# Performance work log

Measured on AMD Instinct MI355X. Metric: run time of the kernel, lower is better.

Reference implementation:

```python
import jax, jax.numpy as jnp
import numpy as np

H, C, OC, WIN = 12, 768, 768, 4
HD = C // H  # 64
B, T = 4, 1024


def setup_inputs() -> dict:
    key = jax.random.key(0)
    ks = jax.random.split(key, 8)
    s = C ** -0.5  # xavier-ish scale for 1x1 convs
    rel_s = HD ** -0.5
    return {
        "x": jax.random.normal(ks[0], (B, C, T), jnp.float32),
        "c": jax.random.normal(ks[1], (B, C, T), jnp.float32),
        "mask": jnp.ones((B, 1, T, T), jnp.float32),
        "wq": jax.random.normal(ks[2], (C, C), jnp.float32) * s,
        "bq": jnp.zeros((C,), jnp.float32),
        "wk": jax.random.normal(ks[3], (C, C), jnp.float32) * s,
        "bk": jnp.zeros((C,), jnp.float32),
        "wv": jax.random.normal(ks[4], (C, C), jnp.float32) * s,
        "bv": jnp.zeros((C,), jnp.float32),
        "wo": jax.random.normal(ks[5], (OC, C), jnp.float32) * s,
        "bo": jnp.zeros((OC,), jnp.float32),
        "emb_rel_k": jax.random.normal(ks[6], (H, 2 * WIN + 1, HD), jnp.float32) * rel_s,
        "emb_rel_v": jax.random.normal(ks[7], (H, 2 * WIN + 1, HD), jnp.float32) * rel_s,
    }


def _conv1x1(x, w, b):
    # Conv1d(kernel_size=1): pointwise linear over channels. x:(b,c,t) w:(o,c)
    return jnp.einsum('oc,bct->bot', w, x) + b[None, :, None]


def _get_rel_emb(emb, t):
    pad = max(t - WIN, 0)
    start = max(WIN + 1 - t, 0)
    emb = jnp.pad(emb, ((0, 0), (pad, pad), (0, 0)))
    return emb[:, start:start + 2 * t - 1, :]


def _rel_to_abs(x):
    # (b,h,t,2t-1) -> (b,h,t,t) via the pad/reshape skew trick
    b, h, t, _ = x.shape
    x = jnp.pad(x, ((0, 0), (0, 0), (0, 0), (0, 1))).reshape(b, h, 2 * t * t)
    x = jnp.pad(x, ((0, 0), (0, 0), (0, t - 1))).reshape(b, h, t + 1, 2 * t - 1)
    return x[:, :, :t, t - 1:]


def _abs_to_rel(x):
    # (b,h,t,t) -> (b,h,t,2t-1) via inverse skew trick
    b, h, t, _ = x.shape
    x = jnp.pad(x, ((0, 0), (0, 0), (0, 0), (0, t - 1))).reshape(b, h, t * (2 * t - 1))
    x = jnp.pad(x, ((0, 0), (0, 0), (t, 0))).reshape(b, h, t, 2 * t)
    return x[:, :, :, 1:]


def reference(x, c, mask, wq, bq, wk, bk, wv, bv, wo, bo, emb_rel_k, emb_rel_v):
    b, _, t = x.shape
    scale = HD ** -0.5
    # (b,c,t) -> (b,h,t,hd)
    q = _conv1x1(x, wq, bq).reshape(b, H, HD, t).transpose(0, 1, 3, 2)
    k = _conv1x1(c, wk, bk).reshape(b, H, HD, t).transpose(0, 1, 3, 2)
    v = _conv1x1(c, wv, bv).reshape(b, H, HD, t).transpose(0, 1, 3, 2)
    scores = jnp.einsum('bhqd,bhkd->bhqk', q, k) * scale  # (b,h,t,t)
    rel_k = _get_rel_emb(emb_rel_k, t)                    # (h,2t-1,d)
    rel_logits = jnp.einsum('bhtd,hmd->bhtm', q, rel_k)   # (b,h,t,2t-1)
    scores = scores + _rel_to_abs(rel_logits) * scale
    scores = jnp.where(mask == 0, jnp.float32(-1e4), scores)
    attn = jax.nn.softmax(scores, axis=-1)
    out = jnp.einsum('bhqk,bhkd->bhqd', attn, v)
    rel_v = _get_rel_emb(emb_rel_v, t)
    out = out + jnp.einsum('bhtm,hmd->bhtd', _abs_to_rel(attn), rel_v)
    out = out.transpose(0, 1, 3, 2).reshape(b, C, t)      # (b,c,t)
    return _conv1x1(out, wo, bo)
```

## Files before the change

kernel.cpp:

```cpp
#include <hip/hip_runtime.h>
#include <stdint.h>
#include <stddef.h>

#define B_ 4
#define T_ 1024
#define C_ 768
#define H_ 12
#define QSCALE 0.18033688011112042f
#define MASKPEN -14427.0f

typedef __attribute__((ext_vector_type(4))) float f32x4;
typedef __attribute__((ext_vector_type(8))) short s16x8;
typedef __attribute__((ext_vector_type(4))) float float4v;

typedef const __attribute__((address_space(1))) uint32_t ga_u32;
typedef __attribute__((address_space(3))) uint32_t lds_u32;

__device__ __forceinline__ float bf2f(uint16_t u) {
    union { uint32_t u; float f; } cv; cv.u = ((uint32_t)u) << 16; return cv.f;
}
__device__ __forceinline__ uint16_t f2bf(float f) {
    union { float f; uint32_t u; } cv; cv.f = f;
    uint32_t u = cv.u;
    return (uint16_t)((u + 0x7FFFu + ((u >> 16) & 1u)) >> 16);
}
__device__ __forceinline__ uint16_t f2bf_trunc(float f) {
    union { float f; uint32_t u; } cv; cv.f = f;
    return (uint16_t)(cv.u >> 16);
}
__device__ __forceinline__ void gload16(const uint16_t* g, uint16_t* l) {
    __builtin_amdgcn_global_load_lds((ga_u32*)g, (lds_u32*)l, 16, 0, 0);
}

__global__ void transpose_bf16_kernel(const float* __restrict__ x,
                                      const float* __restrict__ c,
                                      uint16_t* __restrict__ xT,
                                      uint16_t* __restrict__ cT) {
    __shared__ float tile[32][33];
    const int which = blockIdx.z;
    const int b = blockIdx.y;
    const int t0 = (blockIdx.x % (T_ / 32)) * 32;
    const int c0 = (blockIdx.x / (T_ / 32)) * 32;
    const float* src = (which ? c : x) + (size_t)b * C_ * T_;
    uint16_t* dst = (which ? cT : xT) + (size_t)b * T_ * C_;
    const int lj = threadIdx.x & 31, li = threadIdx.x >> 5;
    #pragma unroll
    for (int i = li; i < 32; i += 8)
        tile[i][lj] = src[(size_t)(c0 + i) * T_ + t0 + lj];
    __syncthreads();
    #pragma unroll
    for (int i = li; i < 32; i += 8)
        dst[(size_t)(t0 + i) * C_ + c0 + lj] = f2bf(tile[lj][i]);
}

__global__ void convert_weights_kernel(const float* __restrict__ wq,
                                       const float* __restrict__ wk,
                                       const float* __restrict__ wv,
                                       const float* __restrict__ wo,
                                       uint16_t* __restrict__ out) {
    const int which = blockIdx.y;
    const float* w = (which == 0) ? wq : (which == 1) ? wk : (which == 2) ? wv : wo;
    const float sc = (which == 0) ? QSCALE : 1.0f;
    uint16_t* dst = out + (size_t)which * C_ * C_;
    const int i = (blockIdx.x * 256 + threadIdx.x) * 4;
    float4v v = *(const float4v*)(w + i);
    uint32_t lo = (uint32_t)f2bf(v[0] * sc) | ((uint32_t)f2bf(v[1] * sc) << 16);
    uint32_t hi = (uint32_t)f2bf(v[2] * sc) | ((uint32_t)f2bf(v[3] * sc) << 16);
    uint32_t* d32 = (uint32_t*)(dst + i);
    d32[0] = lo; d32[1] = hi;
}

__global__ void convert_ek_kernel(const float* __restrict__ ek,
                                  uint16_t* __restrict__ ekb) {
    const int i = blockIdx.x * 256 + threadIdx.x;
    ekb[i] = f2bf(ek[i]);
}

__global__ void mask_bits_kernel(const float* __restrict__ mask,
                                 uint32_t* __restrict__ bits) {
    const size_t i = (size_t)blockIdx.x * 256 + threadIdx.x;
    const float m = mask[i];
    unsigned long long bal = __ballot(m != 0.0f);
    const int lane = threadIdx.x & 63;
    if (lane == 0)       bits[i >> 5] = (uint32_t)bal;
    else if (lane == 32) bits[i >> 5] = (uint32_t)(bal >> 32);
}

__global__ void mask_flags_kernel(const uint32_t* __restrict__ bits,
                                  uint32_t* __restrict__ flags) {
    const int b = blockIdx.y, i0 = blockIdx.x * 64;
    const uint32_t* p = bits + ((size_t)b * T_ + i0) * 32;
    bool ok = true;
    #pragma unroll
    for (int it = 0; it < 8; ++it) ok &= (p[it * 256 + threadIdx.x] == 0xFFFFFFFFu);
    __shared__ int s_ok[4];
    const bool wall = __all(ok);
    if ((threadIdx.x & 63) == 0) s_ok[threadIdx.x >> 6] = wall ? 1 : 0;
    __syncthreads();
    if (threadIdx.x == 0)
        flags[b * 16 + blockIdx.x] = (uint32_t)(s_ok[0] & s_ok[1] & s_ok[2] & s_ok[3]);
}

template <bool OPROJ>
__global__ __launch_bounds__(256, 2)
void gemm_kernel(const uint16_t* __restrict__ xT, const uint16_t* __restrict__ cT,
                 const uint16_t* __restrict__ wb,
                 const float* __restrict__ bq, const float* __restrict__ bk,
                 const float* __restrict__ bv, const float* __restrict__ bo,
                 const uint16_t* __restrict__ attT,
                 uint16_t* __restrict__ Qb, uint16_t* __restrict__ Kb,
                 uint16_t* __restrict__ Vb, float* __restrict__ outp) {
    const int tid = threadIdx.x;
    const int z = blockIdx.z;

    const uint16_t* A; const uint16_t* Bm; const float* bias;
    uint16_t* Cb = nullptr; float* Cf = nullptr;
    int N, ldc; bool bias_col; float bscale = 1.0f;
    if (!OPROJ) {
        const int bat = z & 3, which = z >> 2;
        if (which == 0) {
            A = xT + (size_t)bat * T_ * C_; Bm = wb;                bias = bq;
            Cb = Qb + (size_t)bat * T_ * C_; N = C_; ldc = C_; bias_col = true;
            bscale = QSCALE;
        } else if (which == 1) {
            A = cT + (size_t)bat * T_ * C_; Bm = wb + 1 * C_ * C_;  bias = bk;
            Cb = Kb + (size_t)bat * T_ * C_; N = C_; ldc = C_; bias_col = true;
        } else {
            A = wb + 2 * (size_t)C_ * C_;   Bm = cT + (size_t)(z & 3) * T_ * C_; bias = bv;
            Cb = Vb + (size_t)bat * C_ * T_; N = T_; ldc = T_; bias_col = false;
        }
    } else {
        A = wb + 3 * (size_t)C_ * C_; Bm = attT + (size_t)z * T_ * C_; bias = bo;
        Cf = outp + (size_t)z * C_ * T_; N = T_; ldc = T_; bias_col = false;
    }
    const int tn_cnt = N / 128;
    const int tm = blockIdx.x / tn_cnt, tn = blockIdx.x % tn_cnt;
    const int row0 = tm * 128, col0 = tn * 128;

    __shared__ uint16_t As[128 * 64];
    __shared__ uint16_t Bs[128 * 64];

    const int w = tid >> 6, l = tid & 63;
    const int wr = w & 1, wc = w >> 1;

    const f32x4 zz = {0.f, 0.f, 0.f, 0.f};
    f32x4 acc[4][4];
    #pragma unroll
    for (int i = 0; i < 4; ++i)
        #pragma unroll
        for (int j = 0; j < 4; ++j) acc[i][j] = zz;

    const int sr = tid >> 3, sp = tid & 7;

    for (int kt = 0; kt < 12; ++kt) {
        const int k0 = kt * 64;
        #pragma unroll
        for (int it = 0; it < 4; ++it) {
            const int row = it * 32 + sr;
            const int cch = sp ^ (row & 7);
            gload16(A + (size_t)(row0 + row) * 768 + k0 + cch * 8, &As[row * 64 + sp * 8]);
        }
        #pragma unroll
        for (int it = 0; it < 4; ++it) {
            const int row = it * 32 + sr;
            const int cch = sp ^ (row & 7);
            gload16(Bm + (size_t)(col0 + row) * 768 + k0 + cch * 8, &Bs[row * 64 + sp * 8]);
        }
        __syncthreads();

        #pragma unroll
        for (int kk = 0; kk < 2; ++kk) {
            s16x8 af[4], bf[4];
            #pragma unroll
            for (int i = 0; i < 4; ++i) {
                const int arow = wr * 64 + i * 16 + (l & 15);
                const int ach = (kk * 4 + (l >> 4)) ^ (arow & 7);
                af[i] = *(const s16x8*)(&As[arow * 64 + ach * 8]);
                const int brow = wc * 64 + i * 16 + (l & 15);
                const int bch = (kk * 4 + (l >> 4)) ^ (brow & 7);
                bf[i] = *(const s16x8*)(&Bs[brow * 64 + bch * 8]);
            }
            #pragma unroll
            for (int i = 0; i < 4; ++i)
                #pragma unroll
                for (int j = 0; j < 4; ++j)
                    acc[i][j] = __builtin_amdgcn_mfma_f32_16x16x32_bf16(af[i], bf[j], acc[i][j], 0, 0, 0);
        }
        __syncthreads();
    }

    #pragma unroll
    for (int i = 0; i < 4; ++i) {
        const int rowb = row0 + wr * 64 + i * 16 + ((l >> 4) * 4);
        #pragma unroll
        for (int j = 0; j < 4; ++j) {
            const int col = col0 + wc * 64 + j * 16 + (l & 15);
            const float bc = bias_col ? bias[col] * bscale : 0.f;
            #pragma unroll
            for (int r = 0; r < 4; ++r) {
                const int row = rowb + r;
                const float v = acc[i][j][r] + (bias_col ? bc : bias[row]);
                if (!OPROJ) Cb[(size_t)row * ldc + col] = f2bf(v);
                else        Cf[(size_t)row * ldc + col] = v;
            }
        }
    }
}

__global__ __launch_bounds__(256, 2)
void attn_kernel(const uint16_t* __restrict__ Qb, const uint16_t* __restrict__ Kb,
                 const uint16_t* __restrict__ Vb, const uint32_t* __restrict__ mbits,
                 const uint32_t* __restrict__ flags,
                 const uint16_t* __restrict__ ekb, const float* __restrict__ emb_v,
                 uint16_t* __restrict__ attT) {
    const int i0 = blockIdx.x * 64;
    const int h = blockIdx.y, b = blockIdx.z;
    const int tid = threadIdx.x, w = tid >> 6, l = tid & 63;

    __shared__ uint16_t Ks[2][64 * 64];
    __shared__ uint16_t Vs[2][64 * 64];
    __shared__ uint16_t Ps[64 * 72];
    __shared__ uint16_t Es[16 * 72];
    __shared__ float rk[64 * 9];
    __shared__ float sband[64 * 9];

    const uint16_t* Kbase = Kb + (size_t)b * T_ * C_ + h * 64;
    const uint16_t* Vbase = Vb + (size_t)b * C_ * T_ + (size_t)(h * 64) * T_;
    const int sr = tid >> 3, sp = tid & 7;

    auto stage = [&](int jt, int buf) {
        const int j0s = jt * 64;
        #pragma unroll
        for (int it = 0; it < 2; ++it) {
            const int row = it * 32 + sr;
            const int cch = sp ^ (row & 7);
            gload16(Kbase + (size_t)(j0s + row) * C_ + cch * 8, &Ks[buf][row * 64 + sp * 8]);
        }
        #pragma unroll
        for (int it = 0; it < 2; ++it) {
            const int row = it * 32 + sr;
            const int cch = sp ^ (row & 7);
            gload16(Vbase + (size_t)row * T_ + j0s + cch * 8, &Vs[buf][row * 64 + sp * 8]);
        }
    };

    stage(0, 0);

    s16x8 qf[2];
    {
        const int row = i0 + w * 16 + (l & 15);
        const uint16_t* qp = Qb + ((size_t)(b * T_ + row)) * C_ + h * 64 + (l >> 4) * 8;
        qf[0] = *(const s16x8*)(qp);
        qf[1] = *(const s16x8*)(qp + 32);
    }

    {
        const int idx = tid * 4;
        const int row = idx >> 6, col = idx & 63;
        uint64_t val = 0;
        if (row < 9) val = *(const uint64_t*)(ekb + ((size_t)h * 9 + row) * 64 + col);
        *(uint64_t*)&Es[row * 72 + col] = val;
    }
    for (int t = tid; t < 64 * 9; t += 256) sband[t] = -1e30f;
    __syncthreads();

    {
        f32x4 racc = {0.f, 0.f, 0.f, 0.f};
        #pragma unroll
        for (int kk = 0; kk < 2; ++kk) {
            s16x8 ef = *(const s16x8*)(&Es[(l & 15) * 72 + (l >> 4) * 8 + kk * 32]);
            racc = __builtin_amdgcn_mfma_f32_16x16x32_bf16(qf[kk], ef, racc, 0, 0, 0);
        }
        if ((l & 15) < 9) {
            #pragma unroll
            for (int r = 0; r < 4; ++r)
                rk[(w * 16 + (l >> 4) * 4 + r) * 9 + (l & 15)] = racc[r];
        }
    }

    const bool maskones = (flags[b * 16 + blockIdx.x] != 0);
    const uint32_t* mrow = mbits + (size_t)b * T_ * 32;

    float m[4], lsum[4];
    const f32x4 zz = {0.f, 0.f, 0.f, 0.f};
    f32x4 oacc[4] = {zz, zz, zz, zz};
    #pragma unroll
    for (int r = 0; r < 4; ++r) { m[r] = -1e30f; lsum[r] = 0.f; }

    const int iMin = i0 + w * 16, iMax = iMin + 15;

    for (int jt = 0; jt < 16; ++jt) {
        const int cur = jt & 1;
        if (jt < 15) stage(jt + 1, cur ^ 1);
        const int j0 = jt * 64;

        float sv[4][4];
        #pragma unroll
        for (int tn = 0; tn < 4; ++tn) {
            f32x4 s = zz;
            #pragma unroll
            for (int kk = 0; kk < 2; ++kk) {
                const int krow = tn * 16 + (l & 15);
                const int kch = (kk * 4 + (l >> 4)) ^ (krow & 7);
                s16x8 kf = *(const s16x8*)(&Ks[cur][krow * 64 + kch * 8]);
                s = __builtin_amdgcn_mfma_f32_16x16x32_bf16(qf[kk], kf, s, 0, 0, 0);
            }
            #pragma unroll
            for (int r = 0; r < 4; ++r) sv[tn][r] = s[r];
        }

        const bool bandTile = (j0 <= iMax + 5) && (j0 + 63 >= iMin - 3);
        if (bandTile) {
            #pragma unroll
            for (int tn = 0; tn < 4; ++tn)
                #pragma unroll
                for (int r = 0; r < 4; ++r) {
                    const int iloc = w * 16 + (l >> 4) * 4 + r;
                    const int rr = (j0 + tn * 16 + (l & 15)) - (i0 + iloc) + 3;
                    if ((unsigned)rr < 9u) sv[tn][r] += rk[iloc * 9 + rr];
                }
        }
        if (!maskones) {
            #pragma unroll
            for (int r = 0; r < 4; ++r) {
                const int i = i0 + w * 16 + (l >> 4) * 4 + r;
                const uint32_t m0 = mrow[(size_t)i * 32 + (j0 >> 5)];
                const uint32_t m1 = mrow[(size_t)i * 32 + (j0 >> 5) + 1];
                #pragma unroll
                for (int tn = 0; tn < 4; ++tn) {
                    const uint32_t mw = (tn < 2) ? m0 : m1;
                    const int bit = (tn * 16 + (l & 15)) & 31;
                    if (!((mw >> bit) & 1u)) sv[tn][r] = MASKPEN;
                }
            }
        }
        if (bandTile) {
            #pragma unroll
            for (int tn = 0; tn < 4; ++tn)
                #pragma unroll
                for (int r = 0; r < 4; ++r) {
                    const int iloc = w * 16 + (l >> 4) * 4 + r;
                    const int rr = (j0 + tn * 16 + (l & 15)) - (i0 + iloc) + 3;
                    if ((unsigned)rr < 9u) sband[iloc * 9 + rr] = sv[tn][r];
                }
        }

        float mx[4];
        #pragma unroll
        for (int r = 0; r < 4; ++r)
            mx[r] = fmaxf(fmaxf(sv[0][r], sv[1][r]), fmaxf(sv[2][r], sv[3][r]));
        const bool need = (mx[0] > m[0]) | (mx[1] > m[1]) | (mx[2] > m[2]) | (mx[3] > m[3]);
        if (__any(need)) {
            #pragma unroll
            for (int r = 0; r < 4; ++r) {
                float v = mx[r];
                v = fmaxf(v, __shfl_xor(v, 1));
                v = fmaxf(v, __shfl_xor(v, 2));
                v = fmaxf(v, __shfl_xor(v, 4));
                v = fmaxf(v, __shfl_xor(v, 8));
                const float mn = fmaxf(m[r], v);
                const float alpha = exp2f(m[r] - mn);
                m[r] = mn;
                lsum[r] *= alpha;
                #pragma unroll
                for (int td = 0; td < 4; ++td) oacc[td][r] *= alpha;
            }
        }
        #pragma unroll
        for (int r = 0; r < 4; ++r) {
            #pragma unroll
            for (int tn = 0; tn < 4; ++tn) {
                const float p = exp2f(sv[tn][r] - m[r]);
                sv[tn][r] = p;
                lsum[r] += p;
            }
        }

        #pragma unroll
        for (int tn = 0; tn < 4; ++tn)
            #pragma unroll
            for (int r = 0; r < 4; ++r) {
                const int prow = w * 16 + (l >> 4) * 4 + r;
                Ps[prow * 72 + tn * 16 + (l & 15)] = f2bf_trunc(sv[tn][r]);
            }

        #pragma unroll
        for (int ks = 0; ks < 2; ++ks) {
            const int prow = w * 16 + (l & 15);
            s16x8 pf = *(const s16x8*)(&Ps[prow * 72 + ks * 32 + (l >> 4) * 8]);
            #pragma unroll
            for (int td = 0; td < 4; ++td) {
                const int vrow = td * 16 + (l & 15);
                const int vch = (ks * 4 + (l >> 4)) ^ (vrow & 7);
                s16x8 vf = *(const s16x8*)(&Vs[cur][vrow * 64 + vch * 8]);
                oacc[td] = __builtin_amdgcn_mfma_f32_16x16x32_bf16(pf, vf, oacc[td], 0, 0, 0);
            }
        }
        __syncthreads();
    }

    float invl[4];
    #pragma unroll
    for (int r = 0; r < 4; ++r) {
        float s = lsum[r];
        s += __shfl_xor(s, 1);
        s += __shfl_xor(s, 2);
        s += __shfl_xor(s, 4);
        s += __shfl_xor(s, 8);
        invl[r] = 1.f / s;
    }
    float ab[4][9];
    #pragma unroll
    for (int r = 0; r < 4; ++r) {
        const int iloc = w * 16 + (l >> 4) * 4 + r;
        #pragma unroll
        for (int rr = 0; rr < 9; ++rr)
            ab[r][rr] = exp2f(sband[iloc * 9 + rr] - m[r]) * invl[r];
    }
    #pragma unroll
    for (int td = 0; td < 4; ++td) {
        const int d = td * 16 + (l & 15);
        const float* ev = emb_v + (size_t)h * 9 * 64 + d;
        #pragma unroll
        for (int r = 0; r < 4; ++r) {
            float v = oacc[td][r] * invl[r];
            #pragma unroll
            for (int rr = 0; rr < 9; ++rr) v += ab[r][rr] * ev[rr * 64];
            const int i = i0 + w * 16 + (l >> 4) * 4 + r;
            attT[((size_t)(b * T_ + i)) * C_ + h * 64 + d] = f2bf(v);
        }
    }
}

extern "C" void kernel_launch(void* const* d_in, const int* in_sizes, int n_in,
                              void* d_out, int out_size, void* d_ws, size_t ws_size,
                              hipStream_t stream) {
    const float* x    = (const float*)d_in[0];
    const float* c    = (const float*)d_in[1];
    const float* mask = (const float*)d_in[2];
    const float* wq   = (const float*)d_in[3];
    const float* bq   = (const float*)d_in[4];
    const float* wk   = (const float*)d_in[5];
    const float* bk   = (const float*)d_in[6];
    const float* wv   = (const float*)d_in[7];
    const float* bv   = (const float*)d_in[8];
    const float* wo   = (const float*)d_in[9];
    const float* bo   = (const float*)d_in[10];
    const float* ek   = (const float*)d_in[11];
    const float* ev   = (const float*)d_in[12];
    float* out = (float*)d_out;

    uint8_t* ws = (uint8_t*)d_ws;
    size_t off = 0;
    auto alloc = [&](size_t bytes) {
        uint8_t* p = ws + off;
        off += (bytes + 255) & ~(size_t)255;
        return p;
    };
    uint16_t* xT   = (uint16_t*)alloc((size_t)B_ * T_ * C_ * 2);
    uint16_t* cT   = (uint16_t*)alloc((size_t)B_ * T_ * C_ * 2);
    uint16_t* wb   = (uint16_t*)alloc((size_t)4 * C_ * C_ * 2);
    uint16_t* Qb   = (uint16_t*)alloc((size_t)B_ * T_ * C_ * 2);
    uint16_t* Kb   = (uint16_t*)alloc((size_t)B_ * T_ * C_ * 2);
    uint16_t* Vb   = (uint16_t*)alloc((size_t)B_ * C_ * T_ * 2);
    uint16_t* attT = (uint16_t*)alloc((size_t)B_ * T_ * C_ * 2);
    uint32_t* mbits = (uint32_t*)alloc((size_t)B_ * T_ * 32 * 4);
    uint16_t* ekb  = (uint16_t*)alloc((size_t)H_ * 9 * 64 * 2);
    uint32_t* mflags = (uint32_t*)alloc((size_t)B_ * 16 * 4);

    transpose_bf16_kernel<<<dim3(768, B_, 2), 256, 0, stream>>>(x, c, xT, cT);
    convert_weights_kernel<<<dim3(576, 4), 256, 0, stream>>>(wq, wk, wv, wo, wb);
    convert_ek_kernel<<<dim3(27), 256, 0, stream>>>(ek, ekb);
    mask_bits_kernel<<<dim3((B_ * T_ * T_) / 256), 256, 0, stream>>>(mask, mbits);
    mask_flags_kernel<<<dim3(16, B_), 256, 0, stream>>>(mbits, mflags);
    gemm_kernel<false><<<dim3(48, 1, 12), 256, 0, stream>>>(xT, cT, wb, bq, bk, bv, bo,
                                                            attT, Qb, Kb, Vb, out);
    attn_kernel<<<dim3(T_ / 64, H_, B_), 256, 0, stream>>>(Qb, Kb, Vb, mbits, mflags,
                                                           ekb, ev, attT);
    gemm_kernel<true><<<dim3(48, 1, 4), 256, 0, stream>>>(xT, cT, wb, bq, bk, bv, bo,
                                                          attT, Qb, Kb, Vb, out);
}
```

Measured before the change: 220.9 us.

## Use 128-row query tiles with 512-thread attention blocks and remapped grid

The attention kernel now handles 128 query rows per block with 8 waves sharing each staged K/V tile, which halves the K/V global traffic per query. The grid is flattened to 384 blocks with a remapping that groups batch-head pairs, which may improve L2 locality. The mask-flag granularity is widened to 128 rows to match, and the input transpose kernel is vectorised to float4 loads and 64-bit packed stores. The larger blocks use more LDS and registers per block, so fewer blocks may be resident per CU, and only 384 blocks are launched.

```diff
diff --git a/kernel.cpp b/kernel.cpp
--- a/kernel.cpp
+++ b/kernel.cpp
@@ -39,18 +39,20 @@
     __shared__ float tile[32][33];
     const int which = blockIdx.z;
     const int b = blockIdx.y;
-    const int t0 = (blockIdx.x % (T_ / 32)) * 32;
-    const int c0 = (blockIdx.x / (T_ / 32)) * 32;
+    const int t0 = (blockIdx.x & 31) * 32;
+    const int c0 = (blockIdx.x >> 5) * 32;
     const float* src = (which ? c : x) + (size_t)b * C_ * T_;
     uint16_t* dst = (which ? cT : xT) + (size_t)b * T_ * C_;
-    const int lj = threadIdx.x & 31, li = threadIdx.x >> 5;
-    #pragma unroll
-    for (int i = li; i < 32; i += 8)
-        tile[i][lj] = src[(size_t)(c0 + i) * T_ + t0 + lj];
+    const int li = threadIdx.x >> 3, lj4 = (threadIdx.x & 7) * 4;
+    float4v v = *(const float4v*)(src + (size_t)(c0 + li) * T_ + t0 + lj4);
+    tile[li][lj4 + 0] = v[0]; tile[li][lj4 + 1] = v[1];
+    tile[li][lj4 + 2] = v[2]; tile[li][lj4 + 3] = v[3];
     __syncthreads();
-    #pragma unroll
-    for (int i = li; i < 32; i += 8)
-        dst[(size_t)(t0 + i) * C_ + c0 + lj] = f2bf(tile[lj][i]);
+    const uint64_t pk = (uint64_t)f2bf(tile[lj4 + 0][li])
+                      | ((uint64_t)f2bf(tile[lj4 + 1][li]) << 16)
+                      | ((uint64_t)f2bf(tile[lj4 + 2][li]) << 32)
+                      | ((uint64_t)f2bf(tile[lj4 + 3][li]) << 48);
+    *(uint64_t*)(dst + (size_t)(t0 + li) * C_ + c0 + lj4) = pk;
 }
 
 __global__ void convert_weights_kernel(const float* __restrict__ wq,
@@ -88,17 +90,17 @@
 
 __global__ void mask_flags_kernel(const uint32_t* __restrict__ bits,
                                   uint32_t* __restrict__ flags) {
-    const int b = blockIdx.y, i0 = blockIdx.x * 64;
+    const int b = blockIdx.y, i0 = blockIdx.x * 128;
     const uint32_t* p = bits + ((size_t)b * T_ + i0) * 32;
     bool ok = true;
     #pragma unroll
-    for (int it = 0; it < 8; ++it) ok &= (p[it * 256 + threadIdx.x] == 0xFFFFFFFFu);
+    for (int it = 0; it < 16; ++it) ok &= (p[it * 256 + threadIdx.x] == 0xFFFFFFFFu);
     __shared__ int s_ok[4];
     const bool wall = __all(ok);
     if ((threadIdx.x & 63) == 0) s_ok[threadIdx.x >> 6] = wall ? 1 : 0;
     __syncthreads();
     if (threadIdx.x == 0)
-        flags[b * 16 + blockIdx.x] = (uint32_t)(s_ok[0] & s_ok[1] & s_ok[2] & s_ok[3]);
+        flags[b * 8 + blockIdx.x] = (uint32_t)(s_ok[0] & s_ok[1] & s_ok[2] & s_ok[3]);
 }
 
 template <bool OPROJ>
@@ -207,41 +209,35 @@
     }
 }
 
-__global__ __launch_bounds__(256, 2)
+__global__ __launch_bounds__(512, 4)
 void attn_kernel(const uint16_t* __restrict__ Qb, const uint16_t* __restrict__ Kb,
                  const uint16_t* __restrict__ Vb, const uint32_t* __restrict__ mbits,
                  const uint32_t* __restrict__ flags,
                  const uint16_t* __restrict__ ekb, const float* __restrict__ emb_v,
                  uint16_t* __restrict__ attT) {
-    const int i0 = blockIdx.x * 64;
-    const int h = blockIdx.y, b = blockIdx.z;
+    const int n = blockIdx.x;
+    const int qt = (n >> 3) & 7;
+    const int bh = (n & 7) + 8 * (n >> 6);
+    const int b = bh / 12, h = bh % 12;
+    const int i0 = qt * 128;
     const int tid = threadIdx.x, w = tid >> 6, l = tid & 63;
 
     __shared__ uint16_t Ks[2][64 * 64];
     __shared__ uint16_t Vs[2][64 * 64];
-    __shared__ uint16_t Ps[64 * 72];
+    __shared__ uint16_t Ps[128 * 72];
     __shared__ uint16_t Es[16 * 72];
-    __shared__ float rk[64 * 9];
-    __shared__ float sband[64 * 9];
+    __shared__ float rk[128 * 9];
+    __shared__ float sband[128 * 9];
 
     const uint16_t* Kbase = Kb + (size_t)b * T_ * C_ + h * 64;
     const uint16_t* Vbase = Vb + (size_t)b * C_ * T_ + (size_t)(h * 64) * T_;
-    const int sr = tid >> 3, sp = tid & 7;
+    const int srow = tid >> 3, sp = tid & 7;
+    const int scch = sp ^ (srow & 7);
 
     auto stage = [&](int jt, int buf) {
         const int j0s = jt * 64;
-        #pragma unroll
-        for (int it = 0; it < 2; ++it) {
-            const int row = it * 32 + sr;
-            const int cch = sp ^ (row & 7);
-            gload16(Kbase + (size_t)(j0s + row) * C_ + cch * 8, &Ks[buf][row * 64 + sp * 8]);
-        }
-        #pragma unroll
-        for (int it = 0; it < 2; ++it) {
-            const int row = it * 32 + sr;
-            const int cch = sp ^ (row & 7);
-            gload16(Vbase + (size_t)row * T_ + j0s + cch * 8, &Vs[buf][row * 64 + sp * 8]);
-        }
+        gload16(Kbase + (size_t)(j0s + srow) * C_ + scch * 8, &Ks[buf][srow * 64 + sp * 8]);
+        gload16(Vbase + (size_t)srow * T_ + j0s + scch * 8, &Vs[buf][srow * 64 + sp * 8]);
     };
 
     stage(0, 0);
@@ -255,13 +251,13 @@
     }
 
     {
-        const int idx = tid * 4;
+        const int idx = tid * 2;
         const int row = idx >> 6, col = idx & 63;
-        uint64_t val = 0;
-        if (row < 9) val = *(const uint64_t*)(ekb + ((size_t)h * 9 + row) * 64 + col);
-        *(uint64_t*)&Es[row * 72 + col] = val;
-    }
-    for (int t = tid; t < 64 * 9; t += 256) sband[t] = -1e30f;
+        uint32_t val = 0;
+        if (row < 9) val = *(const uint32_t*)(ekb + ((size_t)h * 9 + row) * 64 + col);
+        *(uint32_t*)&Es[row * 72 + col] = val;
+    }
+    for (int t = tid; t < 128 * 9; t += 512) sband[t] = -1e30f;
     __syncthreads();
 
     {
@@ -278,7 +274,7 @@
         }
     }
 
-    const bool maskones = (flags[b * 16 + blockIdx.x] != 0);
+    const bool maskones = (flags[b * 8 + qt] != 0);
     const uint32_t* mrow = mbits + (size_t)b * T_ * 32;
 
     float m[4], lsum[4];
@@ -466,17 +462,16 @@
     uint16_t* attT = (uint16_t*)alloc((size_t)B_ * T_ * C_ * 2);
     uint32_t* mbits = (uint32_t*)alloc((size_t)B_ * T_ * 32 * 4);
     uint16_t* ekb  = (uint16_t*)alloc((size_t)H_ * 9 * 64 * 2);
-    uint32_t* mflags = (uint32_t*)alloc((size_t)B_ * 16 * 4);
+    uint32_t* mflags = (uint32_t*)alloc((size_t)B_ * 8 * 4);
 
     transpose_bf16_kernel<<<dim3(768, B_, 2), 256, 0, stream>>>(x, c, xT, cT);
     convert_weights_kernel<<<dim3(576, 4), 256, 0, stream>>>(wq, wk, wv, wo, wb);
     convert_ek_kernel<<<dim3(27), 256, 0, stream>>>(ek, ekb);
     mask_bits_kernel<<<dim3((B_ * T_ * T_) / 256), 256, 0, stream>>>(mask, mbits);
-    mask_flags_kernel<<<dim3(16, B_), 256, 0, stream>>>(mbits, mflags);
+    mask_flags_kernel<<<dim3(8, B_), 256, 0, stream>>>(mbits, mflags);
     gemm_kernel<false><<<dim3(48, 1, 12), 256, 0, stream>>>(xT, cT, wb, bq, bk, bv, bo,
                                                             attT, Qb, Kb, Vb, out);
-    attn_kernel<<<dim3(T_ / 64, H_, B_), 256, 0, stream>>>(Qb, Kb, Vb, mbits, mflags,
-                                                           ekb, ev, attT);
+    attn_kernel<<<dim3(384), 512, 0, stream>>>(Qb, Kb, Vb, mbits, mflags, ekb, ev, attT);
     gemm_kernel<true><<<dim3(48, 1, 4), 256, 0, stream>>>(xT, cT, wb, bq, bk, bv, bo,
                                                           attT, Qb, Kb, Vb, out);
 }
```

Result: no change. 224.8 us (+1.7%).
